# Optimization experiments

Measured on AMD Instinct MI355X. Metric: run time of the kernel, lower is better.

The kernel has to match this reference:

```python
import jax, jax.numpy as jnp
import numpy as np

B, S, E = 2, 2048, 2048
H, HKV, D = 16, 8, 64          # num_heads, num_kv_heads, head_dim = E//H//2
NREP = H // HKV
DEPTH = 12
LAMBDA_INIT = 0.8 - 0.6 * float(np.exp(-0.3 * DEPTH))
EPS = 1e-5
SCALE = D ** -0.5
NEG = -1e30


def setup_inputs() -> dict:
    key = jax.random.key(0)
    ks = jax.random.split(key, 10)
    x = jax.random.normal(ks[0], (B, S, E), jnp.float32)
    # rotary tables (seq_len, head_dim/2)
    inv_freq = 1.0 / (10000.0 ** (np.arange(0, D, 2, dtype=np.float32) / D))
    freqs = jnp.asarray(np.outer(np.arange(S, dtype=np.float32), inv_freq), jnp.float32)
    cos, sin = jnp.cos(freqs), jnp.sin(freqs)
    Wq = jax.random.normal(ks[1], (E, E), jnp.float32) * 0.02
    Wk = jax.random.normal(ks[2], (E // NREP, E), jnp.float32) * 0.02
    Wv = jax.random.normal(ks[3], (E // NREP, E), jnp.float32) * 0.02
    Wo = jax.random.normal(ks[4], (E, E), jnp.float32) * 0.02
    lambda_q1 = jax.random.normal(ks[5], (D,), jnp.float32) * 0.1
    lambda_k1 = jax.random.normal(ks[6], (D,), jnp.float32) * 0.1
    lambda_q2 = jax.random.normal(ks[7], (D,), jnp.float32) * 0.1
    lambda_k2 = jax.random.normal(ks[8], (D,), jnp.float32) * 0.1
    subln_w = jnp.ones((2 * D,), jnp.float32)
    return dict(x=x, cos=cos, sin=sin, Wq=Wq, Wk=Wk, Wv=Wv, Wo=Wo,
                lambda_q1=lambda_q1, lambda_k1=lambda_k1,
                lambda_q2=lambda_q2, lambda_k2=lambda_k2, subln_w=subln_w)


def _rotary_interleaved(x, cos, sin):
    # x: (B, S, nh, D); cos/sin: (S, D//2); interleaved pairs (even, odd)
    x1, x2 = x[..., 0::2], x[..., 1::2]
    c = cos[None, :, None, :]
    s = sin[None, :, None, :]
    o1 = x1 * c - x2 * s
    o2 = x1 * s + x2 * c
    return jnp.stack([o1, o2], axis=-1).reshape(x.shape)


def _causal_attn(qh, kh, vcat, mask):
    # qh: (B,S,H,D); kh: (B,S,HKV,D); vcat: (B,S,HKV,2D)
    kr = jnp.repeat(kh, NREP, axis=2)      # GQA repeat -> (B,S,H,D)
    vr = jnp.repeat(vcat, NREP, axis=2)    # (B,S,H,2D)
    scores = jnp.einsum('bqhd,bkhd->bhqk', qh, kr) * SCALE
    scores = jnp.where(mask, scores, NEG)
    p = jax.nn.softmax(scores, axis=-1)
    return jnp.einsum('bhqk,bkhd->bqhd', p, vr)  # (B,S,H,2D)


def reference(x, cos, sin, Wq, Wk, Wv, Wo, lambda_q1, lambda_k1, lambda_q2, lambda_k2, subln_w):
    q = (x @ Wq.T).reshape(B, S, 2 * H, D)
    k = (x @ Wk.T).reshape(B, S, 2 * HKV, D)
    v = (x @ Wv.T).reshape(B, S, HKV, 2, D)
    q = _rotary_interleaved(q, cos, sin).reshape(B, S, H, 2, D)
    k = _rotary_interleaved(k, cos, sin).reshape(B, S, HKV, 2, D)
    vcat = v.reshape(B, S, HKV, 2 * D)  # concat(v1, v2) along last dim
    mask = jnp.tril(jnp.ones((S, S), bool))[None, None]
    a1 = _causal_attn(q[..., 0, :], k[..., 0, :], vcat, mask)
    a2 = _causal_attn(q[..., 1, :], k[..., 1, :], vcat, mask)
    lam = (jnp.exp(jnp.sum(lambda_q1 * lambda_k1))
           - jnp.exp(jnp.sum(lambda_q2 * lambda_k2)) + LAMBDA_INIT)
    a = a1 - lam * a2                      # (B,S,H,2D)
    # RMSNorm over last dim with affine weight, then fixed (1 - lambda_init) scale
    a = a * jax.lax.rsqrt(jnp.mean(a * a, axis=-1, keepdims=True) + EPS) * subln_w
    a = a * (1.0 - LAMBDA_INIT)
    return a.reshape(B, S, E) @ Wo.T
```

## Files before the change

kernel.cpp:

```cpp
#include <hip/hip_runtime.h>
#include <hip/hip_bf16.h>

#define LAMBDA_INIT 0.78360576653162448f

typedef __attribute__((ext_vector_type(8))) short short8;
typedef __attribute__((ext_vector_type(4))) float f32x4;

__device__ __forceinline__ unsigned short f2bf(float f) {
  unsigned int u; __builtin_memcpy(&u, &f, 4);
  u += 0x7fffu + ((u >> 16) & 1u);
  return (unsigned short)(u >> 16);
}
__device__ __forceinline__ unsigned short f2bfn(float f) {
  __hip_bfloat16 h = __float2bfloat16(f);
  unsigned short u; __builtin_memcpy(&u, &h, 2);
  return u;
}
__device__ __forceinline__ short8 cvt8(float4 a, float4 b) {
  short8 s;
  s[0] = (short)f2bf(a.x); s[1] = (short)f2bf(a.y);
  s[2] = (short)f2bf(a.z); s[3] = (short)f2bf(a.w);
  s[4] = (short)f2bf(b.x); s[5] = (short)f2bf(b.y);
  s[6] = (short)f2bf(b.z); s[7] = (short)f2bf(b.w);
  return s;
}

#define GLOAD_LDS16(g, l)                                                     \
  __builtin_amdgcn_global_load_lds(                                           \
      (const __attribute__((address_space(1))) void*)(g),                     \
      (__attribute__((address_space(3))) void*)(l), 16, 0, 0)

__global__ void conv_bf16(const float* __restrict__ in,
                          unsigned short* __restrict__ outp, int n8) {
  const int i = blockIdx.x * 256 + threadIdx.x;
  if (i >= n8) return;
  const float4 a = *(const float4*)(in + (size_t)i * 8);
  const float4 b = *(const float4*)(in + (size_t)i * 8 + 4);
  *(short8*)(outp + (size_t)i * 8) = cvt8(a, b);
}

__global__ void conv_all(const float* __restrict__ x, const float* __restrict__ wq,
                         const float* __restrict__ wk, const float* __restrict__ wv,
                         const float* __restrict__ wo, unsigned short* __restrict__ ws) {
  const int i = blockIdx.x * 256 + threadIdx.x;
  const float* src; size_t so; unsigned short* dst;
  if (i < 1048576)      { src = x;  so = i;           dst = ws; }
  else if (i < 1572864) { src = wq; so = i - 1048576; dst = ws + 8388608; }
  else if (i < 1835008) { src = wk; so = i - 1572864; dst = ws + 12582912; }
  else if (i < 2097152) { src = wv; so = i - 1835008; dst = ws + 14680064; }
  else                  { src = wo; so = i - 2097152; dst = ws + 16777216; }
  const float4 a = *(const float4*)(src + so * 8);
  const float4 b = *(const float4*)(src + so * 8 + 4);
  *(short8*)(dst + so * 8) = cvt8(a, b);
}


__global__ __launch_bounds__(256, 2)
void qkv_bb(const unsigned short* __restrict__ xb,
            const unsigned short* __restrict__ Wqb, const unsigned short* __restrict__ Wkb,
            const unsigned short* __restrict__ Wvb, const float* __restrict__ cosb,
            const float* __restrict__ sinb,
            unsigned short* __restrict__ Qb, unsigned short* __restrict__ Kb,
            unsigned short* __restrict__ Vtb) {
  __shared__ __align__(16) unsigned short As[128 * 64];
  __shared__ __align__(16) unsigned short Bs[128 * 64];
  const int t = threadIdx.x;
  const int wave = t >> 6, lane = t & 63;
  const int l15 = lane & 15, l4 = lane >> 4;
  const int wm = (wave >> 1) * 64, wn = (wave & 1) * 64;
  const int m0 = blockIdx.y * 128, n0 = blockIdx.x * 128;
  const int crow = t >> 3, ccol = (t & 7) * 8;
  const int swc = ccol ^ ((crow & 7) << 3);
  const int rsw = (l15 & 7) << 3;
  const unsigned short* Ag = xb + (size_t)m0 * 2048;

  const unsigned short* Bgh; int ntype;
  if (n0 < 2048)      { Bgh = Wqb + (size_t)n0 * 2048;          ntype = 0; }
  else if (n0 < 3072) { Bgh = Wkb + (size_t)(n0 - 2048) * 2048; ntype = 1; }
  else                { Bgh = Wvb + (size_t)(n0 - 3072) * 2048; ntype = 2; }

  const f32x4 fzero = {0.f, 0.f, 0.f, 0.f};
  f32x4 acc[4][4];
#pragma unroll
  for (int i = 0; i < 4; i++)
#pragma unroll
    for (int j = 0; j < 4; j++) acc[i][j] = fzero;

  for (int kt = 0; kt < 32; ++kt) {
    const int k0 = kt << 6;
    __syncthreads();
#pragma unroll
    for (int j = 0; j < 4; j++) {
      GLOAD_LDS16(Ag + (size_t)(j * 32 + crow) * 2048 + k0 + swc,
                  &As[j * 2048 + wave * 512]);
      GLOAD_LDS16(Bgh + (size_t)(j * 32 + crow) * 2048 + k0 + swc,
                  &Bs[j * 2048 + wave * 512]);
    }
    __syncthreads();
#pragma unroll
    for (int ks = 0; ks < 2; ++ks) {
      const int cb = (ks * 32 + l4 * 8) ^ rsw;
      short8 af[4], bfr[4];
#pragma unroll
      for (int mi = 0; mi < 4; mi++)
        af[mi] = *(const short8*)(&As[(wm + mi * 16 + l15) * 64 + cb]);
#pragma unroll
      for (int ni = 0; ni < 4; ni++)
        bfr[ni] = *(const short8*)(&Bs[(wn + ni * 16 + l15) * 64 + cb]);
#pragma unroll
      for (int mi = 0; mi < 4; mi++)
#pragma unroll
        for (int ni = 0; ni < 4; ni++)
          acc[mi][ni] = __builtin_amdgcn_mfma_f32_16x16x32_bf16(af[mi], bfr[ni], acc[mi][ni], 0, 0, 0);
    }
  }
#pragma unroll
  for (int mi = 0; mi < 4; mi++)
#pragma unroll
    for (int ni = 0; ni < 4; ni++)
#pragma unroll
      for (int r = 0; r < 4; r++) {
        const int m = m0 + wm + mi * 16 + l4 * 4 + r;
        const int n = n0 + wn + ni * 16 + l15;
        float fv = acc[mi][ni][r];
        if (ntype < 2) {
          const int s = m & 2047;
          const int j = (n & 63) >> 1;
          const float c = cosb[s * 32 + j];
          const float sn = sinb[s * 32 + j];
          const float p = __shfl_xor(fv, 1);
          fv = (n & 1) ? (p * sn + fv * c) : (fv * c - p * sn);
        }
        if (ntype == 0)
          Qb[(size_t)m * 2048 + n] = f2bf(fv);
        else if (ntype == 1)
          Kb[(size_t)m * 1024 + (n - 2048)] = f2bf(fv);
        else
          Vtb[((size_t)((m >> 11) * 1024 + (n - 3072))) * 2048 + (m & 2047)] = f2bf(fv);
      }
}

__global__ __launch_bounds__(256, 2)
void o_bb(const unsigned short* __restrict__ Ab, const unsigned short* __restrict__ Wob,
          float* __restrict__ C) {
  __shared__ __align__(16) unsigned short As[128 * 64];
  __shared__ __align__(16) unsigned short Bs[128 * 64];
  const int t = threadIdx.x;
  const int wave = t >> 6, lane = t & 63;
  const int l15 = lane & 15, l4 = lane >> 4;
  const int wm = (wave >> 1) * 64, wn = (wave & 1) * 64;
  const int m0 = blockIdx.y * 128, n0 = blockIdx.x * 128;
  const int crow = t >> 3, ccol = (t & 7) * 8;
  const int swc = ccol ^ ((crow & 7) << 3);
  const int rsw = (l15 & 7) << 3;
  const unsigned short* Ag = Ab + (size_t)m0 * 2048;
  const unsigned short* Bgh = Wob + (size_t)n0 * 2048;

  const f32x4 fzero = {0.f, 0.f, 0.f, 0.f};
  f32x4 acc[4][4];
#pragma unroll
  for (int i = 0; i < 4; i++)
#pragma unroll
    for (int j = 0; j < 4; j++) acc[i][j] = fzero;

  for (int kt = 0; kt < 32; ++kt) {
    const int k0 = kt << 6;
    __syncthreads();
#pragma unroll
    for (int j = 0; j < 4; j++) {
      GLOAD_LDS16(Ag + (size_t)(j * 32 + crow) * 2048 + k0 + swc,
                  &As[j * 2048 + wave * 512]);
      GLOAD_LDS16(Bgh + (size_t)(j * 32 + crow) * 2048 + k0 + swc,
                  &Bs[j * 2048 + wave * 512]);
    }
    __syncthreads();
#pragma unroll
    for (int ks = 0; ks < 2; ++ks) {
      const int cb = (ks * 32 + l4 * 8) ^ rsw;
      short8 af[4], bfr[4];
#pragma unroll
      for (int mi = 0; mi < 4; mi++)
        af[mi] = *(const short8*)(&As[(wm + mi * 16 + l15) * 64 + cb]);
#pragma unroll
      for (int ni = 0; ni < 4; ni++)
        bfr[ni] = *(const short8*)(&Bs[(wn + ni * 16 + l15) * 64 + cb]);
#pragma unroll
      for (int mi = 0; mi < 4; mi++)
#pragma unroll
        for (int ni = 0; ni < 4; ni++)
          acc[mi][ni] = __builtin_amdgcn_mfma_f32_16x16x32_bf16(af[mi], bfr[ni], acc[mi][ni], 0, 0, 0);
    }
  }
#pragma unroll
  for (int mi = 0; mi < 4; mi++)
#pragma unroll
    for (int ni = 0; ni < 4; ni++)
#pragma unroll
      for (int r = 0; r < 4; r++) {
        const int m = m0 + wm + mi * 16 + l4 * 4 + r;
        const int n = n0 + wn + ni * 16 + l15;
        C[(size_t)m * 2048 + n] = acc[mi][ni][r];
      }
}


__global__ __launch_bounds__(256, 2)
void qkv_gemm_f32(const unsigned short* __restrict__ xb,
                  const float* __restrict__ Wq, const float* __restrict__ Wk,
                  const float* __restrict__ Wv, const float* __restrict__ cosb,
                  const float* __restrict__ sinb,
                  unsigned short* __restrict__ Qb, unsigned short* __restrict__ Kb,
                  unsigned short* __restrict__ Vtb) {
  __shared__ __align__(16) unsigned short As[128 * 64];
  __shared__ __align__(16) unsigned short Bs[128 * 72];
  const int t = threadIdx.x;
  const int wave = t >> 6, lane = t & 63;
  const int l15 = lane & 15, l4 = lane >> 4;
  const int wm = (wave >> 1) * 64, wn = (wave & 1) * 64;
  const int m0 = blockIdx.y * 128, n0 = blockIdx.x * 128;
  const int crow = t >> 3, ccol = (t & 7) * 8;
  const unsigned short* Ag = xb + (size_t)m0 * 2048;

  const float* Bg; int ntype;
  if (n0 < 2048)      { Bg = Wq + (size_t)n0 * 2048;          ntype = 0; }
  else if (n0 < 3072) { Bg = Wk + (size_t)(n0 - 2048) * 2048; ntype = 1; }
  else                { Bg = Wv + (size_t)(n0 - 3072) * 2048; ntype = 2; }

  const f32x4 fzero = {0.f, 0.f, 0.f, 0.f};
  f32x4 acc[4][4];
#pragma unroll
  for (int i = 0; i < 4; i++)
#pragma unroll
    for (int j = 0; j < 4; j++) acc[i][j] = fzero;

  float4 rbf[4][2];
#pragma unroll
  for (int i = 0; i < 4; i++) {
    rbf[i][0] = *(const float4*)(Bg + (size_t)(crow + 32 * i) * 2048 + ccol);
    rbf[i][1] = *(const float4*)(Bg + (size_t)(crow + 32 * i) * 2048 + ccol + 4);
  }
  for (int kt = 0; kt < 32; ++kt) {
    const int k0 = kt << 6;
    __syncthreads();
#pragma unroll
    for (int j = 0; j < 4; j++)
      GLOAD_LDS16(Ag + (size_t)(j * 32 + crow) * 2048 + k0 + ccol,
                  &As[j * 2048 + wave * 512]);
#pragma unroll
    for (int i = 0; i < 4; i++)
      *(short8*)(&Bs[(crow + 32 * i) * 72 + ccol]) = cvt8(rbf[i][0], rbf[i][1]);
    __syncthreads();
    if (kt + 1 < 32) {
      const int kn = k0 + 64;
#pragma unroll
      for (int i = 0; i < 4; i++) {
        rbf[i][0] = *(const float4*)(Bg + (size_t)(crow + 32 * i) * 2048 + kn + ccol);
        rbf[i][1] = *(const float4*)(Bg + (size_t)(crow + 32 * i) * 2048 + kn + ccol + 4);
      }
    }
#pragma unroll
    for (int ks = 0; ks < 2; ++ks) {
      short8 af[4], bfr[4];
#pragma unroll
      for (int mi = 0; mi < 4; mi++)
        af[mi] = *(const short8*)(&As[(wm + mi * 16 + l15) * 64 + ks * 32 + l4 * 8]);
#pragma unroll
      for (int ni = 0; ni < 4; ni++)
        bfr[ni] = *(const short8*)(&Bs[(wn + ni * 16 + l15) * 72 + ks * 32 + l4 * 8]);
#pragma unroll
      for (int mi = 0; mi < 4; mi++)
#pragma unroll
        for (int ni = 0; ni < 4; ni++)
          acc[mi][ni] = __builtin_amdgcn_mfma_f32_16x16x32_bf16(af[mi], bfr[ni], acc[mi][ni], 0, 0, 0);
    }
  }
#pragma unroll
  for (int mi = 0; mi < 4; mi++)
#pragma unroll
    for (int ni = 0; ni < 4; ni++)
#pragma unroll
      for (int r = 0; r < 4; r++) {
        const int m = m0 + wm + mi * 16 + l4 * 4 + r;
        const int n = n0 + wn + ni * 16 + l15;
        float fv = acc[mi][ni][r];
        if (ntype < 2) {
          const int s = m & 2047;
          const int j = (n & 63) >> 1;
          const float c = cosb[s * 32 + j];
          const float sn = sinb[s * 32 + j];
          const float p = __shfl_xor(fv, 1);
          fv = (n & 1) ? (p * sn + fv * c) : (fv * c - p * sn);
        }
        if (ntype == 0)
          Qb[(size_t)m * 2048 + n] = f2bf(fv);
        else if (ntype == 1)
          Kb[(size_t)m * 1024 + (n - 2048)] = f2bf(fv);
        else
          Vtb[((size_t)((m >> 11) * 1024 + (n - 3072))) * 2048 + (m & 2047)] = f2bf(fv);
      }
}

__global__ __launch_bounds__(256, 2)
void o_gemm_f32(const unsigned short* __restrict__ Ab, const float* __restrict__ Wo,
                float* __restrict__ C) {
  __shared__ __align__(16) unsigned short As[128 * 64];
  __shared__ __align__(16) unsigned short Bs[128 * 72];
  const int t = threadIdx.x;
  const int wave = t >> 6, lane = t & 63;
  const int l15 = lane & 15, l4 = lane >> 4;
  const int wm = (wave >> 1) * 64, wn = (wave & 1) * 64;
  const int m0 = blockIdx.y * 128, n0 = blockIdx.x * 128;
  const int crow = t >> 3, ccol = (t & 7) * 8;
  const unsigned short* Ag = Ab + (size_t)m0 * 2048;
  const float* Bg = Wo + (size_t)n0 * 2048;

  const f32x4 fzero = {0.f, 0.f, 0.f, 0.f};
  f32x4 acc[4][4];
#pragma unroll
  for (int i = 0; i < 4; i++)
#pragma unroll
    for (int j = 0; j < 4; j++) acc[i][j] = fzero;

  float4 rbf[4][2];
#pragma unroll
  for (int i = 0; i < 4; i++) {
    rbf[i][0] = *(const float4*)(Bg + (size_t)(crow + 32 * i) * 2048 + ccol);
    rbf[i][1] = *(const float4*)(Bg + (size_t)(crow + 32 * i) * 2048 + ccol + 4);
  }
  for (int kt = 0; kt < 32; ++kt) {
    const int k0 = kt << 6;
    __syncthreads();
#pragma unroll
    for (int j = 0; j < 4; j++)
      GLOAD_LDS16(Ag + (size_t)(j * 32 + crow) * 2048 + k0 + ccol,
                  &As[j * 2048 + wave * 512]);
#pragma unroll
    for (int i = 0; i < 4; i++)
      *(short8*)(&Bs[(crow + 32 * i) * 72 + ccol]) = cvt8(rbf[i][0], rbf[i][1]);
    __syncthreads();
    if (kt + 1 < 32) {
      const int kn = k0 + 64;
#pragma unroll
      for (int i = 0; i < 4; i++) {
        rbf[i][0] = *(const float4*)(Bg + (size_t)(crow + 32 * i) * 2048 + kn + ccol);
        rbf[i][1] = *(const float4*)(Bg + (size_t)(crow + 32 * i) * 2048 + kn + ccol + 4);
      }
    }
#pragma unroll
    for (int ks = 0; ks < 2; ++ks) {
      short8 af[4], bfr[4];
#pragma unroll
      for (int mi = 0; mi < 4; mi++)
        af[mi] = *(const short8*)(&As[(wm + mi * 16 + l15) * 64 + ks * 32 + l4 * 8]);
#pragma unroll
      for (int ni = 0; ni < 4; ni++)
        bfr[ni] = *(const short8*)(&Bs[(wn + ni * 16 + l15) * 72 + ks * 32 + l4 * 8]);
#pragma unroll
      for (int mi = 0; mi < 4; mi++)
#pragma unroll
        for (int ni = 0; ni < 4; ni++)
          acc[mi][ni] = __builtin_amdgcn_mfma_f32_16x16x32_bf16(af[mi], bfr[ni], acc[mi][ni], 0, 0, 0);
    }
  }
#pragma unroll
  for (int mi = 0; mi < 4; mi++)
#pragma unroll
    for (int ni = 0; ni < 4; ni++)
#pragma unroll
      for (int r = 0; r < 4; r++) {
        const int m = m0 + wm + mi * 16 + l4 * 4 + r;
        const int n = n0 + wn + ni * 16 + l15;
        C[(size_t)m * 2048 + n] = acc[mi][ni][r];
      }
}

__global__ __launch_bounds__(256, 2)
void attn_kernel(const unsigned short* __restrict__ Q,
                 const unsigned short* __restrict__ Kb,
                 const unsigned short* __restrict__ Vt,
                 unsigned short* __restrict__ Ab,
                 const float* __restrict__ lq1,
                 const float* __restrict__ lk1,
                 const float* __restrict__ lq2,
                 const float* __restrict__ lk2,
                 const float* __restrict__ wsub) {
  const int flat = blockIdx.y * 16 + blockIdx.x;
  const int w = ((flat & 7) << 6) | (flat >> 3);
  const int pi = w & 15;
  const int bh = w >> 4;
  const int b = bh >> 4, h = bh & 15, hk = h >> 1;

  __shared__ __align__(16) unsigned short Ks[2][2][64 * 64];
  __shared__ __align__(16) unsigned short Vs[2][128 * 64];
  __shared__ __align__(16) unsigned short Ps[64 * 64];

  const int t = threadIdx.x;
  const int wave = t >> 6, lane = t & 63;
  const int l15 = lane & 15, l4 = lane >> 4;
  const int crow = t >> 3, ccol = (t & 7) * 8;
  const int swc = ccol ^ ((crow & 7) << 3);

  float s1 = 0.f, s2 = 0.f;
  for (int i = 0; i < 64; i++) {
    s1 += lq1[i] * lk1[i];
    s2 += lq2[i] * lk2[i];
  }
  const float lam = __expf(s1) - __expf(s2) + LAMBDA_INIT;

  float wv[8];
#pragma unroll
  for (int nt = 0; nt < 8; nt++) wv[nt] = wsub[nt * 16 + l15];

  short8 onesf;
#pragma unroll
  for (int j = 0; j < 8; j++) onesf[j] = (l15 == 0) ? (short)0x3F80 : (short)0;

  const f32x4 fzero = {0.f, 0.f, 0.f, 0.f};
  const unsigned short* Kgb = Kb + ((size_t)(b * 2048)) * 1024 + 2 * hk * 64;
  const unsigned short* Vgb = Vt + ((size_t)((b * 8 + hk) * 128)) * 2048;

#define STAGE_KV(KT, BUF)                                                     \
  do {                                                                        \
    const int k0s = (KT) << 6;                                                \
    _Pragma("unroll")                                                         \
    for (int c_ = 0; c_ < 2; c_++)                                            \
      _Pragma("unroll")                                                       \
      for (int i_ = 0; i_ < 2; i_++)                                          \
        GLOAD_LDS16(Kgb + (size_t)(k0s + i_ * 32 + crow) * 1024 + c_ * 64 + swc, \
                    &Ks[BUF][c_][i_ * 2048 + wave * 512]);                    \
    _Pragma("unroll")                                                         \
    for (int i_ = 0; i_ < 4; i_++)                                            \
      GLOAD_LDS16(Vgb + (size_t)(i_ * 32 + crow) * 2048 + k0s + swc,          \
                  &Vs[BUF][i_ * 2048 + wave * 512]);                          \
  } while (0)

  for (int half = 0; half < 2; ++half) {
    const int qi = half ? (31 - pi) : pi;
    const int q0 = qi * 64;
    const int nkt = qi + 1;

    short8 qf[2][2];
#pragma unroll
    for (int c = 0; c < 2; c++)
#pragma unroll
      for (int ks = 0; ks < 2; ks++)
        qf[c][ks] = *(const short8*)(Q + ((size_t)(b * 2048 + q0 + wave * 16 + l15)) * 2048
                                       + (2 * h + c) * 64 + ks * 32 + l4 * 8);

    f32x4 accO[2][8];
    f32x4 accL[2];
#pragma unroll
    for (int c = 0; c < 2; c++) {
      accL[c] = fzero;
#pragma unroll
      for (int nt = 0; nt < 8; nt++) accO[c][nt] = fzero;
    }

    __syncthreads();
    STAGE_KV(0, 0);

    for (int kt = 0; kt < nkt; ++kt) {
      const int cur = kt & 1;
      __syncthreads();
      if (kt + 1 < nkt) STAGE_KV(kt + 1, cur ^ 1);

      const unsigned short* Ksb0 = &Ks[cur][0][0];
      const unsigned short* Ksb1 = &Ks[cur][1][0];
      const unsigned short* Vsb  = &Vs[cur][0];
      const bool diag = (kt == qi);

      short8 pf[2][2];
      const int rbase = wave * 16 + l4 * 4;
      const int sw0 = (rbase & 7) << 3;
#pragma unroll
      for (int c = 0; c < 2; c++) {
        const unsigned short* Ksb = c ? Ksb1 : Ksb0;
#pragma unroll
        for (int ct = 0; ct < 4; ct++) {
          const int kr = ct * 16 + l15;
          const int ksw = (kr & 7) << 3;
          const short8 kb0 = *(const short8*)(&Ksb[kr * 64 + ((l4 * 8) ^ ksw)]);
          const short8 kb1 = *(const short8*)(&Ksb[kr * 64 + ((32 + l4 * 8) ^ ksw)]);
          f32x4 z = fzero;
          z = __builtin_amdgcn_mfma_f32_16x16x32_bf16(qf[c][0], kb0, z, 0, 0, 0);
          z = __builtin_amdgcn_mfma_f32_16x16x32_bf16(qf[c][1], kb1, z, 0, 0, 0);
          float e[4];
#pragma unroll
          for (int r = 0; r < 4; r++)
            e[r] = exp2f(fmaf(z[r], 0.18033688011112042f, -23.083120654223414f));
          if (diag) {
#pragma unroll
            for (int r = 0; r < 4; r++)
              if ((ct * 16 + l15) > (rbase + r)) e[r] = 0.f;
          }
          const int colsw = (ct * 16 + l15) ^ sw0;
#pragma unroll
          for (int r = 0; r < 4; r++)
            Ps[(rbase + r) * 64 + (colsw ^ (r << 3))] = f2bfn(e[r]);
        }
        {
          const int prow = wave * 16 + l15;
          const int psw = (l15 & 7) << 3;
#pragma unroll
          for (int ks = 0; ks < 2; ks++)
            pf[c][ks] = *(const short8*)(&Ps[prow * 64 + ((ks * 32 + l4 * 8) ^ psw)]);
        }
      }

      __builtin_amdgcn_s_setprio(1);
#pragma unroll
      for (int nt = 0; nt < 8; nt++) {
        const int vrow = nt * 16 + l15;
        const int vsw = (vrow & 7) << 3;
        const short8 v0 = *(const short8*)(&Vsb[vrow * 64 + ((l4 * 8) ^ vsw)]);
        const short8 v1 = *(const short8*)(&Vsb[vrow * 64 + ((32 + l4 * 8) ^ vsw)]);
        accO[0][nt] = __builtin_amdgcn_mfma_f32_16x16x32_bf16(pf[0][0], v0, accO[0][nt], 0, 0, 0);
        accO[0][nt] = __builtin_amdgcn_mfma_f32_16x16x32_bf16(pf[0][1], v1, accO[0][nt], 0, 0, 0);
        accO[1][nt] = __builtin_amdgcn_mfma_f32_16x16x32_bf16(pf[1][0], v0, accO[1][nt], 0, 0, 0);
        accO[1][nt] = __builtin_amdgcn_mfma_f32_16x16x32_bf16(pf[1][1], v1, accO[1][nt], 0, 0, 0);
      }
#pragma unroll
      for (int c = 0; c < 2; c++) {
        accL[c] = __builtin_amdgcn_mfma_f32_16x16x32_bf16(pf[c][0], onesf, accL[c], 0, 0, 0);
        accL[c] = __builtin_amdgcn_mfma_f32_16x16x32_bf16(pf[c][1], onesf, accL[c], 0, 0, 0);
      }
      __builtin_amdgcn_s_setprio(0);
    }

#pragma unroll
    for (int r = 0; r < 4; r++) {
      const float l1 = __shfl(accL[0][r], lane & 48);
      const float l2 = __shfl(accL[1][r], lane & 48);
      const float i1 = 1.f / fmaxf(l1, 1e-30f);
      const float i2 = lam / fmaxf(l2, 1e-30f);
      float av[8], ss = 0.f;
#pragma unroll
      for (int nt = 0; nt < 8; nt++) {
        const float a = accO[0][nt][r] * i1 - accO[1][nt][r] * i2;
        av[nt] = a;
        ss += a * a;
      }
#pragma unroll
      for (int off = 1; off < 16; off <<= 1) ss += __shfl_xor(ss, off, 16);
      const float sca = rsqrtf(ss * (1.f / 128.f) + 1e-5f) * (1.f - LAMBDA_INIT);
      const int qrow = q0 + wave * 16 + l4 * 4 + r;
      unsigned short* Ao = Ab + ((size_t)(b * 2048 + qrow)) * 2048 + h * 128;
#pragma unroll
      for (int nt = 0; nt < 8; nt++)
        Ao[nt * 16 + l15] = f2bfn(av[nt] * sca * wv[nt]);
    }
  }
#undef STAGE_KV
}

extern "C" void kernel_launch(void* const* d_in, const int* in_sizes, int n_in,
                              void* d_out, int out_size, void* d_ws, size_t ws_size,
                              hipStream_t stream) {
  const float* x    = (const float*)d_in[0];
  const float* cosb = (const float*)d_in[1];
  const float* sinb = (const float*)d_in[2];
  const float* Wq   = (const float*)d_in[3];
  const float* Wk   = (const float*)d_in[4];
  const float* Wv   = (const float*)d_in[5];
  const float* Wo   = (const float*)d_in[6];
  const float* lq1  = (const float*)d_in[7];
  const float* lk1  = (const float*)d_in[8];
  const float* lq2  = (const float*)d_in[9];
  const float* lk2  = (const float*)d_in[10];
  const float* wsub = (const float*)d_in[11];
  float* out = (float*)d_out;

  unsigned short* XA  = (unsigned short*)d_ws;
  unsigned short* Kb  = (unsigned short*)d_out;
  unsigned short* Vtb = Kb + (size_t)4096 * 1024;
  unsigned short* Qb  = Vtb + (size_t)2 * 1024 * 2048;

  dim3 blk(256);
  if (ws_size >= (size_t)41943040) {
    unsigned short* Wqb = XA + 8388608;
    unsigned short* Wkb = XA + 12582912;
    unsigned short* Wvb = XA + 14680064;
    unsigned short* Wob = XA + 16777216;
    conv_all<<<10240, blk, 0, stream>>>(x, Wq, Wk, Wv, Wo, XA);
    qkv_bb<<<dim3(32, 32), blk, 0, stream>>>(XA, Wqb, Wkb, Wvb, cosb, sinb, Qb, Kb, Vtb);
    attn_kernel<<<dim3(16, 32), blk, 0, stream>>>(Qb, Kb, Vtb, XA, lq1, lk1, lq2, lk2, wsub);
    o_bb<<<dim3(16, 32), blk, 0, stream>>>(XA, Wob, out);
  } else {
    conv_bf16<<<4096, blk, 0, stream>>>(x, XA, 1048576);
    qkv_gemm_f32<<<dim3(32, 32), blk, 0, stream>>>(XA, Wq, Wk, Wv, cosb, sinb, Qb, Kb, Vtb);
    attn_kernel<<<dim3(16, 32), blk, 0, stream>>>(Qb, Kb, Vtb, XA, lq1, lk1, lq2, lk2, wsub);
    o_gemm_f32<<<dim3(16, 32), blk, 0, stream>>>(XA, Wo, out);
  }
}
```

Baseline: 366.4 us.

## Double-buffer LDS tiles in QKV and output-projection GEMMs

Both bf16 GEMM kernels now use two LDS buffers for the A and B tiles. Each iteration issues the direct global-to-LDS loads for the next K tile into the spare buffer, then runs the MFMAs on the current one. This overlaps global memory latency with compute and drops from two barriers per K step to one. In exchange, LDS per block doubles to 64 KB, and the overlap depends on the compiler not inserting a conservative wait on the pending loads before the LDS reads.

```diff
diff --git a/kernel.cpp b/kernel.cpp
--- a/kernel.cpp
+++ b/kernel.cpp
@@ -62,8 +62,8 @@
             const float* __restrict__ sinb,
             unsigned short* __restrict__ Qb, unsigned short* __restrict__ Kb,
             unsigned short* __restrict__ Vtb) {
-  __shared__ __align__(16) unsigned short As[128 * 64];
-  __shared__ __align__(16) unsigned short Bs[128 * 64];
+  __shared__ __align__(16) unsigned short As[2][128 * 64];
+  __shared__ __align__(16) unsigned short Bs[2][128 * 64];
   const int t = threadIdx.x;
   const int wave = t >> 6, lane = t & 63;
   const int l15 = lane & 15, l4 = lane >> 4;
@@ -79,6 +79,18 @@
   else if (n0 < 3072) { Bgh = Wkb + (size_t)(n0 - 2048) * 2048; ntype = 1; }
   else                { Bgh = Wvb + (size_t)(n0 - 3072) * 2048; ntype = 2; }
 
+#define STAGE_AB(KT, BUF)                                                     \
+  do {                                                                        \
+    const int k0s = (KT) << 6;                                                \
+    _Pragma("unroll")                                                         \
+    for (int j_ = 0; j_ < 4; j_++) {                                          \
+      GLOAD_LDS16(Ag + (size_t)(j_ * 32 + crow) * 2048 + k0s + swc,           \
+                  &As[BUF][j_ * 2048 + wave * 512]);                          \
+      GLOAD_LDS16(Bgh + (size_t)(j_ * 32 + crow) * 2048 + k0s + swc,          \
+                  &Bs[BUF][j_ * 2048 + wave * 512]);                          \
+    }                                                                         \
+  } while (0)
+
   const f32x4 fzero = {0.f, 0.f, 0.f, 0.f};
   f32x4 acc[4][4];
 #pragma unroll
@@ -86,27 +98,23 @@
 #pragma unroll
     for (int j = 0; j < 4; j++) acc[i][j] = fzero;
 
+  STAGE_AB(0, 0);
   for (int kt = 0; kt < 32; ++kt) {
-    const int k0 = kt << 6;
+    const int cur = kt & 1;
     __syncthreads();
-#pragma unroll
-    for (int j = 0; j < 4; j++) {
-      GLOAD_LDS16(Ag + (size_t)(j * 32 + crow) * 2048 + k0 + swc,
-                  &As[j * 2048 + wave * 512]);
-      GLOAD_LDS16(Bgh + (size_t)(j * 32 + crow) * 2048 + k0 + swc,
-                  &Bs[j * 2048 + wave * 512]);
-    }
-    __syncthreads();
+    if (kt + 1 < 32) STAGE_AB(kt + 1, cur ^ 1);
+    const unsigned short* Asb = &As[cur][0];
+    const unsigned short* Bsb = &Bs[cur][0];
 #pragma unroll
     for (int ks = 0; ks < 2; ++ks) {
       const int cb = (ks * 32 + l4 * 8) ^ rsw;
       short8 af[4], bfr[4];
 #pragma unroll
       for (int mi = 0; mi < 4; mi++)
-        af[mi] = *(const short8*)(&As[(wm + mi * 16 + l15) * 64 + cb]);
+        af[mi] = *(const short8*)(&Asb[(wm + mi * 16 + l15) * 64 + cb]);
 #pragma unroll
       for (int ni = 0; ni < 4; ni++)
-        bfr[ni] = *(const short8*)(&Bs[(wn + ni * 16 + l15) * 64 + cb]);
+        bfr[ni] = *(const short8*)(&Bsb[(wn + ni * 16 + l15) * 64 + cb]);
 #pragma unroll
       for (int mi = 0; mi < 4; mi++)
 #pragma unroll
@@ -114,6 +122,7 @@
           acc[mi][ni] = __builtin_amdgcn_mfma_f32_16x16x32_bf16(af[mi], bfr[ni], acc[mi][ni], 0, 0, 0);
     }
   }
+#undef STAGE_AB
 #pragma unroll
   for (int mi = 0; mi < 4; mi++)
 #pragma unroll
@@ -143,8 +152,8 @@
 __global__ __launch_bounds__(256, 2)
 void o_bb(const unsigned short* __restrict__ Ab, const unsigned short* __restrict__ Wob,
           float* __restrict__ C) {
-  __shared__ __align__(16) unsigned short As[128 * 64];
-  __shared__ __align__(16) unsigned short Bs[128 * 64];
+  __shared__ __align__(16) unsigned short As[2][128 * 64];
+  __shared__ __align__(16) unsigned short Bs[2][128 * 64];
   const int t = threadIdx.x;
   const int wave = t >> 6, lane = t & 63;
   const int l15 = lane & 15, l4 = lane >> 4;
@@ -156,6 +165,18 @@
   const unsigned short* Ag = Ab + (size_t)m0 * 2048;
   const unsigned short* Bgh = Wob + (size_t)n0 * 2048;
 
+#define STAGE_AB(KT, BUF)                                                     \
+  do {                                                                        \
+    const int k0s = (KT) << 6;                                                \
+    _Pragma("unroll")                                                         \
+    for (int j_ = 0; j_ < 4; j_++) {                                          \
+      GLOAD_LDS16(Ag + (size_t)(j_ * 32 + crow) * 2048 + k0s + swc,           \
+                  &As[BUF][j_ * 2048 + wave * 512]);                          \
+      GLOAD_LDS16(Bgh + (size_t)(j_ * 32 + crow) * 2048 + k0s + swc,          \
+                  &Bs[BUF][j_ * 2048 + wave * 512]);                          \
+    }                                                                         \
+  } while (0)
+
   const f32x4 fzero = {0.f, 0.f, 0.f, 0.f};
   f32x4 acc[4][4];
 #pragma unroll
@@ -163,27 +184,23 @@
 #pragma unroll
     for (int j = 0; j < 4; j++) acc[i][j] = fzero;
 
+  STAGE_AB(0, 0);
   for (int kt = 0; kt < 32; ++kt) {
-    const int k0 = kt << 6;
+    const int cur = kt & 1;
     __syncthreads();
-#pragma unroll
-    for (int j = 0; j < 4; j++) {
-      GLOAD_LDS16(Ag + (size_t)(j * 32 + crow) * 2048 + k0 + swc,
-                  &As[j * 2048 + wave * 512]);
-      GLOAD_LDS16(Bgh + (size_t)(j * 32 + crow) * 2048 + k0 + swc,
-                  &Bs[j * 2048 + wave * 512]);
-    }
-    __syncthreads();
+    if (kt + 1 < 32) STAGE_AB(kt + 1, cur ^ 1);
+    const unsigned short* Asb = &As[cur][0];
+    const unsigned short* Bsb = &Bs[cur][0];
 #pragma unroll
     for (int ks = 0; ks < 2; ++ks) {
       const int cb = (ks * 32 + l4 * 8) ^ rsw;
       short8 af[4], bfr[4];
 #pragma unroll
       for (int mi = 0; mi < 4; mi++)
-        af[mi] = *(const short8*)(&As[(wm + mi * 16 + l15) * 64 + cb]);
+        af[mi] = *(const short8*)(&Asb[(wm + mi * 16 + l15) * 64 + cb]);
 #pragma unroll
       for (int ni = 0; ni < 4; ni++)
-        bfr[ni] = *(const short8*)(&Bs[(wn + ni * 16 + l15) * 64 + cb]);
+        bfr[ni] = *(const short8*)(&Bsb[(wn + ni * 16 + l15) * 64 + cb]);
 #pragma unroll
       for (int mi = 0; mi < 4; mi++)
 #pragma unroll
@@ -191,6 +208,7 @@
           acc[mi][ni] = __builtin_amdgcn_mfma_f32_16x16x32_bf16(af[mi], bfr[ni], acc[mi][ni], 0, 0, 0);
     }
   }
+#undef STAGE_AB
 #pragma unroll
   for (int mi = 0; mi < 4; mi++)
 #pragma unroll
```

Measured after the change: 368.8 us. No clear change (+0.7%).
